# Kernel optimization log

Measured on AMD Instinct MI355X. Metric: run time of the kernel, lower is better.

The kernel has to match this reference:

```python
import jax, jax.numpy as jnp
import numpy as np

U, I, D = 100000, 150000, 64
N = U + I
E = 1250000
KEEP_RATE = 0.8


def setup_inputs() -> dict:
    key = jax.random.key(0)
    k1, k2, k3, k4, k5, k6 = jax.random.split(key, 6)
    row = jax.random.randint(k1, (E,), 0, N, dtype=jnp.int32)
    col = jax.random.randint(k2, (E,), 0, N, dtype=jnp.int32)
    adj_values = jax.random.uniform(k3, (E,), dtype=jnp.float32)
    # edge dropout mask: floor(rand + keep_rate) in {0,1}, exactly as SpAdjEdgeDrop
    edge_mask = jnp.floor(jax.random.uniform(k4, (E,), dtype=jnp.float32) + KEEP_RATE)
    user_embeds = jax.random.normal(k5, (U, D), dtype=jnp.float32)
    item_embeds = jax.random.normal(k6, (I, D), dtype=jnp.float32)
    return {
        "row": row,
        "col": col,
        "adj_values": adj_values,
        "edge_mask": edge_mask,
        "user_embeds": user_embeds,
        "item_embeds": item_embeds,
        "layer_num": 3,
    }


def reference(row, col, adj_values, edge_mask, user_embeds, item_embeds, layer_num):
    user_num = user_embeds.shape[0]
    n_nodes = user_num + item_embeds.shape[0]
    # edge-dropped sparse values (mask==0 edges contribute nothing to spmm)
    vals = adj_values * edge_mask  # [E]
    embeds = jnp.concatenate([user_embeds, item_embeds], axis=0)  # [N, D]
    acc = embeds
    cur = embeds
    for _ in range(layer_num):
        # spmm: out[r] += vals[e] * cur[c] for each edge e=(r,c)
        msgs = vals[:, None] * cur[col]  # [E, D] gather
        cur = jax.ops.segment_sum(msgs, row, num_segments=n_nodes)  # [N, D] scatter-add
        acc = acc + cur
    out = acc / (layer_num + 1)
    return out[:user_num], out[user_num:]
```

## Files before the change

### kernel.cpp

```cpp
#include <hip/hip_runtime.h>


#define U_NODES 100000
#define N_NODES 250000
#define DIM4 16
#define E_EDGES 1250000
#define TILE_ROWS 1024
#define NT 245
#define NB 1024
#define GSZ (NB * 256)
#define BSEG 1280
#define TCAP 8192

typedef unsigned short u16;

__device__ __forceinline__ float bf2f(u16 h) {
    return __uint_as_float(((unsigned)h) << 16);
}
__device__ __forceinline__ u16 f2bf(float f) {
    unsigned u = __float_as_uint(f);
    u += 0x7fffu + ((u >> 16) & 1u);
    return (u16)(u >> 16);
}
__device__ __forceinline__ ushort4 gat(const u16* __restrict__ base, int node, int part) {
    return ((const ushort4*)(base + ((size_t)node << 6)))[part];
}
__device__ __forceinline__ void fma4(float4& s, float v, ushort4 h) {
    s.x += v * bf2f(h.x);
    s.y += v * bf2f(h.y);
    s.z += v * bf2f(h.z);
    s.w += v * bf2f(h.w);
}

__global__ void lgcn_part(const float4* __restrict__ user4,
                          const float4* __restrict__ item4,
                          u16* __restrict__ e0b,
                          const int* __restrict__ row,
                          const int* __restrict__ col,
                          const float* __restrict__ adj,
                          const float* __restrict__ mask,
                          int* __restrict__ OFF,
                          int2* __restrict__ staging) {
    __shared__ int lhist[256];
    __shared__ int lscan[256];
    __shared__ int loff[256];
    __shared__ int lcur[256];
    const int t = threadIdx.x;
    const int b = blockIdx.x;
    const int g0 = b * 256 + t;

    lhist[t] = 0;
    __syncthreads();

    int r0 = -1, r1 = -1, r2 = -1, r3 = -1, r4 = -1;
    float v0 = 0.f, v1 = 0.f, v2 = 0.f, v3 = 0.f, v4 = 0.f;
    {
        int e = g0;
        if (e < E_EDGES) { float m = mask[e]; if (m != 0.f) { r0 = row[e]; v0 = m; atomicAdd(&lhist[r0 >> 10], 1); } }
        e += GSZ;
        if (e < E_EDGES) { float m = mask[e]; if (m != 0.f) { r1 = row[e]; v1 = m; atomicAdd(&lhist[r1 >> 10], 1); } }
        e += GSZ;
        if (e < E_EDGES) { float m = mask[e]; if (m != 0.f) { r2 = row[e]; v2 = m; atomicAdd(&lhist[r2 >> 10], 1); } }
        e += GSZ;
        if (e < E_EDGES) { float m = mask[e]; if (m != 0.f) { r3 = row[e]; v3 = m; atomicAdd(&lhist[r3 >> 10], 1); } }
        e += GSZ;
        if (e < E_EDGES) { float m = mask[e]; if (m != 0.f) { r4 = row[e]; v4 = m; atomicAdd(&lhist[r4 >> 10], 1); } }
    }
    __syncthreads();

    int v = lhist[t];
    lscan[t] = v;
    __syncthreads();
    for (int off = 1; off < 256; off <<= 1) {
        int u = (t >= off) ? lscan[t - off] : 0;
        __syncthreads();
        if (t >= off) lscan[t] += u;
        __syncthreads();
    }
    loff[t] = lscan[t] - v;
    lcur[t] = 0;
    __syncthreads();

    OFF[b * 256 + t] = loff[t];

    const int CONV = N_NODES * 8;
    for (int i = g0; i < CONV; i += GSZ) {
        const int uc = U_NODES * 8;
        const float4* src = (i < uc) ? (user4 + 2 * (long)i)
                                     : (item4 + 2 * (long)(i - uc));
        float4 a = src[0];
        float4 bb = src[1];
        int4 o;
        o.x = (int)((unsigned)f2bf(a.x) | ((unsigned)f2bf(a.y) << 16));
        o.y = (int)((unsigned)f2bf(a.z) | ((unsigned)f2bf(a.w) << 16));
        o.z = (int)((unsigned)f2bf(bb.x) | ((unsigned)f2bf(bb.y) << 16));
        o.w = (int)((unsigned)f2bf(bb.z) | ((unsigned)f2bf(bb.w) << 16));
        ((int4*)e0b)[i] = o;
    }
    __syncthreads();

    {
        int e = g0;
        if (r0 >= 0) { int bkt = r0 >> 10; int rank = loff[bkt] + atomicAdd(&lcur[bkt], 1);
            staging[(size_t)b * BSEG + rank] = make_int2(((r0 & 1023) << 18) | col[e], __float_as_int(adj[e] * v0)); }
        e += GSZ;
        if (r1 >= 0) { int bkt = r1 >> 10; int rank = loff[bkt] + atomicAdd(&lcur[bkt], 1);
            staging[(size_t)b * BSEG + rank] = make_int2(((r1 & 1023) << 18) | col[e], __float_as_int(adj[e] * v1)); }
        e += GSZ;
        if (r2 >= 0) { int bkt = r2 >> 10; int rank = loff[bkt] + atomicAdd(&lcur[bkt], 1);
            staging[(size_t)b * BSEG + rank] = make_int2(((r2 & 1023) << 18) | col[e], __float_as_int(adj[e] * v2)); }
        e += GSZ;
        if (r3 >= 0) { int bkt = r3 >> 10; int rank = loff[bkt] + atomicAdd(&lcur[bkt], 1);
            staging[(size_t)b * BSEG + rank] = make_int2(((r3 & 1023) << 18) | col[e], __float_as_int(adj[e] * v3)); }
        e += GSZ;
        if (r4 >= 0) { int bkt = r4 >> 10; int rank = loff[bkt] + atomicAdd(&lcur[bkt], 1);
            staging[(size_t)b * BSEG + rank] = make_int2(((r4 & 1023) << 18) | col[e], __float_as_int(adj[e] * v4)); }
    }
}

__global__ void lgcn_build(const int* __restrict__ OFF,
                           const int2* __restrict__ staging,
                           int2* __restrict__ rowdesc,
                           int2* __restrict__ csr) {
    __shared__ int lcount[TILE_ROWS];
    __shared__ int lstart[TILE_ROWS];
    __shared__ int lcur[TILE_ROWS];
    __shared__ int lscan[256];
    const int i = blockIdx.x;
    const int t = threadIdx.x;

    lcount[t] = 0; lcount[t + 256] = 0; lcount[t + 512] = 0; lcount[t + 768] = 0;
    __syncthreads();

    const int b0 = t, b1 = t + 256, b2 = t + 512, b3 = t + 768;
    const int o0 = OFF[(b0 << 8) + i], n0 = OFF[(b0 << 8) + i + 1] - o0;
    const int o1 = OFF[(b1 << 8) + i], n1 = OFF[(b1 << 8) + i + 1] - o1;
    const int o2 = OFF[(b2 << 8) + i], n2 = OFF[(b2 << 8) + i + 1] - o2;
    const int o3 = OFF[(b3 << 8) + i], n3 = OFF[(b3 << 8) + i + 1] - o3;
    const int2* run0 = staging + (size_t)b0 * BSEG + o0;
    const int2* run1 = staging + (size_t)b1 * BSEG + o1;
    const int2* run2 = staging + (size_t)b2 * BSEG + o2;
    const int2* run3 = staging + (size_t)b3 * BSEG + o3;

    for (int j = 0; j < n0; ++j) atomicAdd(&lcount[((unsigned)run0[j].x) >> 18], 1);
    for (int j = 0; j < n1; ++j) atomicAdd(&lcount[((unsigned)run1[j].x) >> 18], 1);
    for (int j = 0; j < n2; ++j) atomicAdd(&lcount[((unsigned)run2[j].x) >> 18], 1);
    for (int j = 0; j < n3; ++j) atomicAdd(&lcount[((unsigned)run3[j].x) >> 18], 1);
    __syncthreads();

    int d0 = lcount[4 * t + 0], d1 = lcount[4 * t + 1];
    int d2 = lcount[4 * t + 2], d3 = lcount[4 * t + 3];
    int p0 = (d0 + 3) & ~3, p1 = (d1 + 3) & ~3, p2 = (d2 + 3) & ~3, p3 = (d3 + 3) & ~3;
    int s = p0 + p1 + p2 + p3;
    lscan[t] = s;
    __syncthreads();
    for (int off = 1; off < 256; off <<= 1) {
        int u = (t >= off) ? lscan[t - off] : 0;
        __syncthreads();
        if (t >= off) lscan[t] += u;
        __syncthreads();
    }
    int pos = i * TCAP + lscan[t] - s;
    const int rbase = (i << 10) + 4 * t;
    if (rbase + 0 < N_NODES) rowdesc[rbase + 0] = make_int2(pos, d0);
    lstart[4 * t + 0] = pos; lcur[4 * t + 0] = pos; pos += p0;
    if (rbase + 1 < N_NODES) rowdesc[rbase + 1] = make_int2(pos, d1);
    lstart[4 * t + 1] = pos; lcur[4 * t + 1] = pos; pos += p1;
    if (rbase + 2 < N_NODES) rowdesc[rbase + 2] = make_int2(pos, d2);
    lstart[4 * t + 2] = pos; lcur[4 * t + 2] = pos; pos += p2;
    if (rbase + 3 < N_NODES) rowdesc[rbase + 3] = make_int2(pos, d3);
    lstart[4 * t + 3] = pos; lcur[4 * t + 3] = pos;
    __syncthreads();

    for (int j = 0; j < n0; ++j) { int2 rec = run0[j]; int rw = ((unsigned)rec.x) >> 18;
        csr[atomicAdd(&lcur[rw], 1)] = make_int2(rec.x & 0x3FFFF, rec.y); }
    for (int j = 0; j < n1; ++j) { int2 rec = run1[j]; int rw = ((unsigned)rec.x) >> 18;
        csr[atomicAdd(&lcur[rw], 1)] = make_int2(rec.x & 0x3FFFF, rec.y); }
    for (int j = 0; j < n2; ++j) { int2 rec = run2[j]; int rw = ((unsigned)rec.x) >> 18;
        csr[atomicAdd(&lcur[rw], 1)] = make_int2(rec.x & 0x3FFFF, rec.y); }
    for (int j = 0; j < n3; ++j) { int2 rec = run3[j]; int rw = ((unsigned)rec.x) >> 18;
        csr[atomicAdd(&lcur[rw], 1)] = make_int2(rec.x & 0x3FFFF, rec.y); }
}

template <bool LAST>
__global__ void lgcn_pull(const int2* __restrict__ rowdesc,
                          const int2* __restrict__ csr,
                          const u16*  __restrict__ curb,
                          const u16*  __restrict__ e0b,
                          const u16*  __restrict__ e1b,
                          u16*        __restrict__ outb,
                          float4*     __restrict__ out) {
    int tid = blockIdx.x * blockDim.x + threadIdx.x;
    int r = tid >> 4;
    int part = tid & 15;
    if (r >= N_NODES) return;
    int2 rd = rowdesc[r];
    int start = rd.x;
    int pend  = start + ((rd.y + 3) & ~3);
    float4 s = make_float4(0.f, 0.f, 0.f, 0.f);
    int e = start;
    for (; e + 8 <= pend; e += 8) {
        int4 ca = *(const int4*)(csr + e);
        int4 cb = *(const int4*)(csr + e + 2);
        int4 cc = *(const int4*)(csr + e + 4);
        int4 cd = *(const int4*)(csr + e + 6);
        ushort4 h0 = gat(curb, ca.x, part);
        ushort4 h1 = gat(curb, ca.z, part);
        ushort4 h2 = gat(curb, cb.x, part);
        ushort4 h3 = gat(curb, cb.z, part);
        ushort4 h4 = gat(curb, cc.x, part);
        ushort4 h5 = gat(curb, cc.z, part);
        ushort4 h6 = gat(curb, cd.x, part);
        ushort4 h7 = gat(curb, cd.z, part);
        fma4(s, __int_as_float(ca.y), h0);
        fma4(s, __int_as_float(ca.w), h1);
        fma4(s, __int_as_float(cb.y), h2);
        fma4(s, __int_as_float(cb.w), h3);
        fma4(s, __int_as_float(cc.y), h4);
        fma4(s, __int_as_float(cc.w), h5);
        fma4(s, __int_as_float(cd.y), h6);
        fma4(s, __int_as_float(cd.w), h7);
    }
    if (e < pend) {
        int4 ca = *(const int4*)(csr + e);
        int4 cb = *(const int4*)(csr + e + 2);
        ushort4 h0 = gat(curb, ca.x, part);
        ushort4 h1 = gat(curb, ca.z, part);
        ushort4 h2 = gat(curb, cb.x, part);
        ushort4 h3 = gat(curb, cb.z, part);
        fma4(s, __int_as_float(ca.y), h0);
        fma4(s, __int_as_float(ca.w), h1);
        fma4(s, __int_as_float(cb.y), h2);
        fma4(s, __int_as_float(cb.w), h3);
    }
    size_t oi = (size_t)r * DIM4 + part;
    if (LAST) {
        ushort4 a0 = ((const ushort4*)e0b)[oi];
        ushort4 a1 = ((const ushort4*)e1b)[oi];
        ushort4 a2 = ((const ushort4*)curb)[oi];
        out[oi] = make_float4(
            (s.x + bf2f(a0.x) + bf2f(a1.x) + bf2f(a2.x)) * 0.25f,
            (s.y + bf2f(a0.y) + bf2f(a1.y) + bf2f(a2.y)) * 0.25f,
            (s.z + bf2f(a0.z) + bf2f(a1.z) + bf2f(a2.z)) * 0.25f,
            (s.w + bf2f(a0.w) + bf2f(a1.w) + bf2f(a2.w)) * 0.25f);
    } else {
        ((ushort4*)outb)[oi] = make_ushort4(f2bf(s.x), f2bf(s.y), f2bf(s.z), f2bf(s.w));
    }
}

extern "C" void kernel_launch(void* const* d_in, const int* in_sizes, int n_in,
                              void* d_out, int out_size, void* d_ws, size_t ws_size,
                              hipStream_t stream) {
    const int*   row  = (const int*)d_in[0];
    const int*   col  = (const int*)d_in[1];
    const float* adj  = (const float*)d_in[2];
    const float* mask = (const float*)d_in[3];
    const float4* user4 = (const float4*)d_in[4];
    const float4* item4 = (const float4*)d_in[5];

    float4* acc = (float4*)d_out;

    const size_t bemb_bytes = (size_t)N_NODES * 64 * sizeof(u16);
    char* p = (char*)d_ws;
    u16* e0b = (u16*)p;  p += bemb_bytes;
    u16* e1b = (u16*)p;  p += bemb_bytes;
    u16* e2b = (u16*)p;  p += bemb_bytes;
    int* OFF   = (int*)p;  p += (size_t)NB * 256 * 4;
    int2* staging = (int2*)p;  p += (size_t)NB * BSEG * 8;
    int2* rowdesc = (int2*)p;  p += ((size_t)N_NODES * 8 + 63) & ~63ul;
    int2* csr     = (int2*)p;
    const size_t csr_bytes = (size_t)NT * TCAP * 8;

    const int BLK = 256;
    const long node_vec4 = (long)N_NODES * DIM4;
    const int  grid_pull = (int)((node_vec4 + BLK - 1) / BLK);

    hipMemsetAsync(csr, 0, csr_bytes, stream);
    lgcn_part<<<NB, BLK, 0, stream>>>(user4, item4, e0b, row, col, adj, mask,
                                      OFF, staging);
    lgcn_build<<<NT, BLK, 0, stream>>>(OFF, staging, rowdesc, csr);

    lgcn_pull<false><<<grid_pull, BLK, 0, stream>>>(rowdesc, csr, e0b, nullptr, nullptr, e1b, nullptr);
    lgcn_pull<false><<<grid_pull, BLK, 0, stream>>>(rowdesc, csr, e1b, nullptr, nullptr, e2b, nullptr);
    lgcn_pull<true ><<<grid_pull, BLK, 0, stream>>>(rowdesc, csr, e2b, e0b, e1b, nullptr, acc);
}
```

Baseline: 297.3 us.

## Double bucketing blocks, pack staging records early, drop redundant barrier

Doubles the number of blocks in the bucketing pass so each thread handles three edges instead of five, and shrinks the per-block staging segment to match. Staging records (local row, col, scaled value) are now built during the first pass, so col/adj are not re-read after the conversion loop, and the barrier between the conversion loop and the staging scatter is removed. The build kernel now walks eight runs per thread instead of four and drops an unused shared array. The intent is more parallelism and less latency in preprocessing, at the cost of twice as many small runs to merge in the build step and more live registers.

```diff
diff --git a/kernel.cpp b/kernel.cpp
--- a/kernel.cpp
+++ b/kernel.cpp
@@ -7,9 +7,9 @@
 #define E_EDGES 1250000
 #define TILE_ROWS 1024
 #define NT 245
-#define NB 1024
+#define NB 2048
 #define GSZ (NB * 256)
-#define BSEG 1280
+#define BSEG 768
 #define TCAP 8192
 
 typedef unsigned short u16;
@@ -52,19 +52,36 @@
     lhist[t] = 0;
     __syncthreads();
 
-    int r0 = -1, r1 = -1, r2 = -1, r3 = -1, r4 = -1;
-    float v0 = 0.f, v1 = 0.f, v2 = 0.f, v3 = 0.f, v4 = 0.f;
+    int bk0 = -1, bk1 = -1, bk2 = -1;
+    int2 rc0 = make_int2(0, 0), rc1 = make_int2(0, 0), rc2 = make_int2(0, 0);
     {
         int e = g0;
-        if (e < E_EDGES) { float m = mask[e]; if (m != 0.f) { r0 = row[e]; v0 = m; atomicAdd(&lhist[r0 >> 10], 1); } }
+        if (e < E_EDGES) {
+            float m = mask[e];
+            if (m != 0.f) {
+                int r = row[e]; bk0 = r >> 10;
+                rc0 = make_int2(((r & 1023) << 18) | col[e], __float_as_int(adj[e] * m));
+                atomicAdd(&lhist[bk0], 1);
+            }
+        }
         e += GSZ;
-        if (e < E_EDGES) { float m = mask[e]; if (m != 0.f) { r1 = row[e]; v1 = m; atomicAdd(&lhist[r1 >> 10], 1); } }
+        if (e < E_EDGES) {
+            float m = mask[e];
+            if (m != 0.f) {
+                int r = row[e]; bk1 = r >> 10;
+                rc1 = make_int2(((r & 1023) << 18) | col[e], __float_as_int(adj[e] * m));
+                atomicAdd(&lhist[bk1], 1);
+            }
+        }
         e += GSZ;
-        if (e < E_EDGES) { float m = mask[e]; if (m != 0.f) { r2 = row[e]; v2 = m; atomicAdd(&lhist[r2 >> 10], 1); } }
-        e += GSZ;
-        if (e < E_EDGES) { float m = mask[e]; if (m != 0.f) { r3 = row[e]; v3 = m; atomicAdd(&lhist[r3 >> 10], 1); } }
-        e += GSZ;
-        if (e < E_EDGES) { float m = mask[e]; if (m != 0.f) { r4 = row[e]; v4 = m; atomicAdd(&lhist[r4 >> 10], 1); } }
+        if (e < E_EDGES) {
+            float m = mask[e];
+            if (m != 0.f) {
+                int r = row[e]; bk2 = r >> 10;
+                rc2 = make_int2(((r & 1023) << 18) | col[e], __float_as_int(adj[e] * m));
+                atomicAdd(&lhist[bk2], 1);
+            }
+        }
     }
     __syncthreads();
 
@@ -97,24 +114,18 @@
         o.w = (int)((unsigned)f2bf(bb.z) | ((unsigned)f2bf(bb.w) << 16));
         ((int4*)e0b)[i] = o;
     }
-    __syncthreads();
-
-    {
-        int e = g0;
-        if (r0 >= 0) { int bkt = r0 >> 10; int rank = loff[bkt] + atomicAdd(&lcur[bkt], 1);
-            staging[(size_t)b * BSEG + rank] = make_int2(((r0 & 1023) << 18) | col[e], __float_as_int(adj[e] * v0)); }
-        e += GSZ;
-        if (r1 >= 0) { int bkt = r1 >> 10; int rank = loff[bkt] + atomicAdd(&lcur[bkt], 1);
-            staging[(size_t)b * BSEG + rank] = make_int2(((r1 & 1023) << 18) | col[e], __float_as_int(adj[e] * v1)); }
-        e += GSZ;
-        if (r2 >= 0) { int bkt = r2 >> 10; int rank = loff[bkt] + atomicAdd(&lcur[bkt], 1);
-            staging[(size_t)b * BSEG + rank] = make_int2(((r2 & 1023) << 18) | col[e], __float_as_int(adj[e] * v2)); }
-        e += GSZ;
-        if (r3 >= 0) { int bkt = r3 >> 10; int rank = loff[bkt] + atomicAdd(&lcur[bkt], 1);
-            staging[(size_t)b * BSEG + rank] = make_int2(((r3 & 1023) << 18) | col[e], __float_as_int(adj[e] * v3)); }
-        e += GSZ;
-        if (r4 >= 0) { int bkt = r4 >> 10; int rank = loff[bkt] + atomicAdd(&lcur[bkt], 1);
-            staging[(size_t)b * BSEG + rank] = make_int2(((r4 & 1023) << 18) | col[e], __float_as_int(adj[e] * v4)); }
+
+    if (bk0 >= 0) {
+        int rank = loff[bk0] + atomicAdd(&lcur[bk0], 1);
+        staging[(size_t)b * BSEG + rank] = rc0;
+    }
+    if (bk1 >= 0) {
+        int rank = loff[bk1] + atomicAdd(&lcur[bk1], 1);
+        staging[(size_t)b * BSEG + rank] = rc1;
+    }
+    if (bk2 >= 0) {
+        int rank = loff[bk2] + atomicAdd(&lcur[bk2], 1);
+        staging[(size_t)b * BSEG + rank] = rc2;
     }
 }
 
@@ -123,7 +134,6 @@
                            int2* __restrict__ rowdesc,
                            int2* __restrict__ csr) {
     __shared__ int lcount[TILE_ROWS];
-    __shared__ int lstart[TILE_ROWS];
     __shared__ int lcur[TILE_ROWS];
     __shared__ int lscan[256];
     const int i = blockIdx.x;
@@ -132,20 +142,20 @@
     lcount[t] = 0; lcount[t + 256] = 0; lcount[t + 512] = 0; lcount[t + 768] = 0;
     __syncthreads();
 
-    const int b0 = t, b1 = t + 256, b2 = t + 512, b3 = t + 768;
-    const int o0 = OFF[(b0 << 8) + i], n0 = OFF[(b0 << 8) + i + 1] - o0;
-    const int o1 = OFF[(b1 << 8) + i], n1 = OFF[(b1 << 8) + i + 1] - o1;
-    const int o2 = OFF[(b2 << 8) + i], n2 = OFF[(b2 << 8) + i + 1] - o2;
-    const int o3 = OFF[(b3 << 8) + i], n3 = OFF[(b3 << 8) + i + 1] - o3;
-    const int2* run0 = staging + (size_t)b0 * BSEG + o0;
-    const int2* run1 = staging + (size_t)b1 * BSEG + o1;
-    const int2* run2 = staging + (size_t)b2 * BSEG + o2;
-    const int2* run3 = staging + (size_t)b3 * BSEG + o3;
-
-    for (int j = 0; j < n0; ++j) atomicAdd(&lcount[((unsigned)run0[j].x) >> 18], 1);
-    for (int j = 0; j < n1; ++j) atomicAdd(&lcount[((unsigned)run1[j].x) >> 18], 1);
-    for (int j = 0; j < n2; ++j) atomicAdd(&lcount[((unsigned)run2[j].x) >> 18], 1);
-    for (int j = 0; j < n3; ++j) atomicAdd(&lcount[((unsigned)run3[j].x) >> 18], 1);
+    int o[8], n[8];
+#pragma unroll
+    for (int k = 0; k < 8; ++k) {
+        const int bb = t + (k << 8);
+        o[k] = OFF[(bb << 8) + i];
+        n[k] = OFF[(bb << 8) + i + 1] - o[k];
+    }
+
+#pragma unroll
+    for (int k = 0; k < 8; ++k) {
+        const int2* run = staging + (size_t)(t + (k << 8)) * BSEG + o[k];
+        for (int j = 0; j < n[k]; ++j)
+            atomicAdd(&lcount[((unsigned)run[j].x) >> 18], 1);
+    }
     __syncthreads();
 
     int d0 = lcount[4 * t + 0], d1 = lcount[4 * t + 1];
@@ -163,23 +173,24 @@
     int pos = i * TCAP + lscan[t] - s;
     const int rbase = (i << 10) + 4 * t;
     if (rbase + 0 < N_NODES) rowdesc[rbase + 0] = make_int2(pos, d0);
-    lstart[4 * t + 0] = pos; lcur[4 * t + 0] = pos; pos += p0;
+    lcur[4 * t + 0] = pos; pos += p0;
     if (rbase + 1 < N_NODES) rowdesc[rbase + 1] = make_int2(pos, d1);
-    lstart[4 * t + 1] = pos; lcur[4 * t + 1] = pos; pos += p1;
+    lcur[4 * t + 1] = pos; pos += p1;
     if (rbase + 2 < N_NODES) rowdesc[rbase + 2] = make_int2(pos, d2);
-    lstart[4 * t + 2] = pos; lcur[4 * t + 2] = pos; pos += p2;
+    lcur[4 * t + 2] = pos; pos += p2;
     if (rbase + 3 < N_NODES) rowdesc[rbase + 3] = make_int2(pos, d3);
-    lstart[4 * t + 3] = pos; lcur[4 * t + 3] = pos;
-    __syncthreads();
-
-    for (int j = 0; j < n0; ++j) { int2 rec = run0[j]; int rw = ((unsigned)rec.x) >> 18;
-        csr[atomicAdd(&lcur[rw], 1)] = make_int2(rec.x & 0x3FFFF, rec.y); }
-    for (int j = 0; j < n1; ++j) { int2 rec = run1[j]; int rw = ((unsigned)rec.x) >> 18;
-        csr[atomicAdd(&lcur[rw], 1)] = make_int2(rec.x & 0x3FFFF, rec.y); }
-    for (int j = 0; j < n2; ++j) { int2 rec = run2[j]; int rw = ((unsigned)rec.x) >> 18;
-        csr[atomicAdd(&lcur[rw], 1)] = make_int2(rec.x & 0x3FFFF, rec.y); }
-    for (int j = 0; j < n3; ++j) { int2 rec = run3[j]; int rw = ((unsigned)rec.x) >> 18;
-        csr[atomicAdd(&lcur[rw], 1)] = make_int2(rec.x & 0x3FFFF, rec.y); }
+    lcur[4 * t + 3] = pos;
+    __syncthreads();
+
+#pragma unroll
+    for (int k = 0; k < 8; ++k) {
+        const int2* run = staging + (size_t)(t + (k << 8)) * BSEG + o[k];
+        for (int j = 0; j < n[k]; ++j) {
+            int2 rec = run[j];
+            int rw = ((unsigned)rec.x) >> 18;
+            csr[atomicAdd(&lcur[rw], 1)] = make_int2(rec.x & 0x3FFFF, rec.y);
+        }
+    }
 }
 
 template <bool LAST>
```

New measurement: 304.1 us. 2.3% more time.
